# Kernel optimization log

Hardware: AMD Instinct MI355X
Metric: run time of the kernel (lower is better)

The kernel has to match this reference:

```python
import jax, jax.numpy as jnp
import numpy as np

NUM_ROI = 400
N_GRAPHS = 128
N_NODES = NUM_ROI * N_GRAPHS            # 51200
N_EDGES = N_NODES * 40                  # 2048000
EMB = [128, 128]
BN_EPS = 1e-5


def mish(x):
    return x * jnp.tanh(jax.nn.softplus(x))


def gcn_conv(x, row, col, ew, W, b, n_nodes):
    """PyG GCNConv: h = XW; add self-loops (w=1); sym-normalize; scatter-add; + bias."""
    h = x @ W                                            # [N, out]
    loops = jnp.arange(n_nodes, dtype=row.dtype)
    row_ = jnp.concatenate([row, loops])
    col_ = jnp.concatenate([col, loops])
    ew_ = jnp.concatenate([ew, jnp.ones((n_nodes,), ew.dtype)])
    deg = jax.ops.segment_sum(ew_, col_, num_segments=n_nodes)
    dinv = jnp.where(deg > 0, jax.lax.rsqrt(deg), 0.0)
    norm = dinv[row_] * ew_ * dinv[col_]                 # [E+N]
    msg = norm[:, None] * h[row_]                        # gather + scale
    out = jax.ops.segment_sum(msg, col_, num_segments=n_nodes)
    return out + b


def setup_inputs() -> dict:
    key = jax.random.key(0)
    ks = jax.random.split(key, 16)
    inp = {
        "x": jax.random.normal(ks[0], (N_NODES, NUM_ROI), jnp.float32),
        "edge_index": jax.random.randint(ks[1], (2, N_EDGES), 0, N_NODES, jnp.int64)
        if jax.config.jax_enable_x64 else jax.random.randint(ks[1], (2, N_EDGES), 0, N_NODES, jnp.int32),
        "edge_attr": jax.random.uniform(ks[2], (N_EDGES,), jnp.float32),
        "batch": jnp.repeat(jnp.arange(N_GRAPHS), NUM_ROI),
        "conv1_w": jax.random.normal(ks[3], (NUM_ROI, EMB[0]), jnp.float32) * 0.05,
        "conv1_b": jax.random.normal(ks[4], (EMB[0],), jnp.float32) * 0.05,
        "conv2_w": jax.random.normal(ks[5], (EMB[0], EMB[1]), jnp.float32) * 0.05,
        "conv2_b": jax.random.normal(ks[6], (EMB[1],), jnp.float32) * 0.05,
        "ro_w": jax.random.normal(ks[7], (EMB[1], 8), jnp.float32) * 0.05,
        "ro_b": jax.random.normal(ks[8], (8,), jnp.float32) * 0.05,
        "fc1_w": jax.random.normal(ks[9], (8 * NUM_ROI, NUM_ROI), jnp.float32) * 0.02,
        "fc1_b": jax.random.normal(ks[10], (NUM_ROI,), jnp.float32) * 0.02,
        "bn_gamma": jnp.ones((NUM_ROI,), jnp.float32),
        "bn_beta": jnp.zeros((NUM_ROI,), jnp.float32),
        "fc2_w": jax.random.normal(ks[11], (NUM_ROI, 2), jnp.float32) * 0.05,
        "fc2_b": jax.random.normal(ks[12], (2,), jnp.float32) * 0.05,
    }
    return inp


def reference(x, edge_index, edge_attr, batch,
              conv1_w, conv1_b, conv2_w, conv2_b,
              ro_w, ro_b, fc1_w, fc1_b, bn_gamma, bn_beta, fc2_w, fc2_b):
    n = x.shape[0]
    row, col = edge_index[0], edge_index[1]
    h = mish(gcn_conv(x, row, col, edge_attr, conv1_w, conv1_b, n))
    h = mish(gcn_conv(h, row, col, edge_attr, conv2_w, conv2_b, n))
    out = mish(h @ ro_w + ro_b)                          # [N, 8]
    feats = out.reshape(-1, NUM_ROI * 8)                 # [B, 3200]
    z = feats @ fc1_w + fc1_b                            # [B, 400]
    # BatchNorm1d (training mode: batch statistics, biased variance)
    mu = jnp.mean(z, axis=0)
    var = jnp.mean((z - mu) ** 2, axis=0)
    zn = (z - mu) * jax.lax.rsqrt(var + BN_EPS) * bn_gamma + bn_beta
    logits = mish(zn) @ fc2_w + fc2_b                    # [B, 2]
    return logits
```

## Files before the change

### kernel.cpp

```cpp
#include <hip/hip_runtime.h>
#include <hip/hip_fp16.h>
#include <math.h>

#define NN 51200
#define NE 2048000
#define F 128
#define NB 1000
#define EPB 2048
#define NBKT 200
#define ECAP 12288

typedef _Float16 half8 __attribute__((ext_vector_type(8)));
typedef float floatx4 __attribute__((ext_vector_type(4)));

__device__ __forceinline__ float mish_f(float x) {
  if (x > 20.0f) return x;
  float e = __expf(x);
  float w = 1.0f + e;
  w = w * w;
  return x * (w - 1.0f) / (w + 1.0f);
}

__global__ __launch_bounds__(256) void k_ic(const int* __restrict__ ei, unsigned* __restrict__ G,
                                            const float* __restrict__ W1, const float* __restrict__ W2,
                                            _Float16* __restrict__ Wt1, _Float16* __restrict__ Wt2,
                                            float* __restrict__ z) {
  int bid = blockIdx.x, t = threadIdx.x;
  if (bid < NB) {
    __shared__ unsigned hist[NBKT];
    for (int i = t; i < NBKT; i += 256) hist[i] = 0u;
    __syncthreads();
    int base = bid * EPB;
    for (int it = 0; it < EPB; it += 256) {
      int dst = ei[NE + base + it + t];
      atomicAdd(&hist[dst >> 8], 1u);
    }
    __syncthreads();
    for (int i = t; i < NBKT; i += 256) G[(size_t)i * NB + bid] = hist[i];
  } else {
    int idx = (bid - NB) * 256 + t;
    if (idx < 51200) {
      int k = idx >> 7, n = idx & 127;
      Wt1[n * 400 + k] = (_Float16)W1[idx];
      z[idx] = 0.0f;
    } else {
      int i2 = idx - 51200;
      int k = i2 >> 7, n = i2 & 127;
      Wt2[n * 128 + k] = (_Float16)W2[i2];
    }
  }
}

__global__ __launch_bounds__(64) void k_bscan(unsigned* __restrict__ G, unsigned* __restrict__ btot) {
  int b = blockIdx.x, l = threadIdx.x;
  unsigned base = (unsigned)l * 16;
  unsigned loc[16];
  unsigned s = 0;
#pragma unroll
  for (int i = 0; i < 16; ++i) {
    unsigned idx = base + i;
    unsigned x = (idx < NB) ? G[(size_t)b * NB + idx] : 0u;
    loc[i] = s;
    s += x;
  }
  unsigned run = s;
#pragma unroll
  for (int off = 1; off < 64; off <<= 1) {
    unsigned y = __shfl_up(run, off);
    if (l >= off) run += y;
  }
  unsigned excl = run - s;
#pragma unroll
  for (int i = 0; i < 16; ++i) {
    unsigned idx = base + i;
    if (idx < NB) G[(size_t)b * NB + idx] = excl + loc[i];
  }
  if (l == 63) btot[b] = run;
}

__global__ __launch_bounds__(256) void k_cscat(const int* __restrict__ ei, const float* __restrict__ ew,
                                               const unsigned* __restrict__ G,
                                               uint2* __restrict__ E) {
  __shared__ unsigned cur[NBKT];
  int blk = blockIdx.x, t = threadIdx.x;
  for (int i = t; i < NBKT; i += 256) cur[i] = (unsigned)i * ECAP + G[(size_t)i * NB + blk];
  __syncthreads();
  int base = blk * EPB;
  for (int it = 0; it < EPB; it += 256) {
    int e = base + it + t;
    int dst = ei[NE + e];
    int src = ei[e];
    float w = ew[e];
    unsigned pos = atomicAdd(&cur[dst >> 8], 1u);
    E[pos] = make_uint2((unsigned)src | ((unsigned)(dst & 255) << 16), __float_as_uint(w));
  }
}

__global__ __launch_bounds__(512) void k_fprep(const uint2* __restrict__ E, const unsigned* __restrict__ btot,
                                               int2* __restrict__ bounds, float* __restrict__ dinv,
                                               unsigned* __restrict__ csr) {
  __shared__ unsigned lc[256];
  __shared__ float ld[256];
  __shared__ int curs[256];
  __shared__ int ws4[4];
  __shared__ int starts[256];
  int b = blockIdx.x, t = threadIdx.x;
  if (t < 256) {
    lc[t] = 0u;
    ld[t] = 0.f;
  }
  __syncthreads();
  unsigned e0 = (unsigned)b * ECAP, e1 = e0 + btot[b];
  for (unsigned e = e0 + t; e < e1; e += 512) {
    uint2 v = E[e];
    unsigned node = (v.x >> 16) & 255u;
    atomicAdd(&lc[node], 1u);
    atomicAdd(&ld[node], __uint_as_float(v.y));
  }
  __syncthreads();
  if (t < 256) {
    int lane = t & 63, wid = t >> 6;
    int cv = (int)lc[t];
    int x = cv;
#pragma unroll
    for (int off = 1; off < 64; off <<= 1) {
      int y = __shfl_up(x, off);
      if (lane >= off) x += y;
    }
    if (lane == 63) ws4[wid] = x;
    __syncthreads();
    int woff = 0;
    for (int k = 0; k < wid; ++k) woff += ws4[k];
    int start = (int)e0 + woff + x - cv;
    bounds[b * 256 + t] = make_int2(start, start + cv);
    dinv[b * 256 + t] = rsqrtf(ld[t] + 1.0f);
    curs[t] = start;
    starts[t] = start;
  } else {
    __syncthreads();
  }
  __syncthreads();
  for (unsigned e = e0 + t; e < e1; e += 512) {
    uint2 v = E[e];
    unsigned node = (v.x >> 16) & 255u;
    unsigned src = v.x & 0xFFFFu;
    int p = atomicAdd(&curs[node], 1);
    unsigned pk = src | ((unsigned)__half_as_ushort(__float2half_rn(__uint_as_float(v.y))) << 16);
    csr[p] = pk;
  }
  (void)starts;
}

template <bool A_IS_F32>
__global__ __launch_bounds__(256) void k_gemm16(const void* __restrict__ Av,
                                                const _Float16* __restrict__ Wt,
                                                const float* __restrict__ dinv,
                                                __half* __restrict__ C, int K) {
  __shared__ _Float16 As[128][40];
  __shared__ _Float16 Bs[128][40];
  int t = threadIdx.x;
  int bm = blockIdx.x * 128;
  int w = t >> 6, l = t & 63, rr = l & 15, q = l >> 4;
  int si = t >> 1, sj = (t & 1) * 16;

  floatx4 acc[2][8];
#pragma unroll
  for (int a = 0; a < 2; ++a)
#pragma unroll
    for (int b = 0; b < 8; ++b) acc[a][b] = (floatx4){0.f, 0.f, 0.f, 0.f};

  for (int k0 = 0; k0 < K; k0 += 32) {
    if (A_IS_F32) {
      const float* A = (const float*)Av;
      half8 h0, h1;
      if (k0 + sj < K) {
        const float* ap = A + (size_t)(bm + si) * K + k0 + sj;
        float4 v0 = *(const float4*)(ap + 0);
        float4 v1 = *(const float4*)(ap + 4);
        float4 v2 = *(const float4*)(ap + 8);
        float4 v3 = *(const float4*)(ap + 12);
        h0 = (half8){(_Float16)v0.x, (_Float16)v0.y, (_Float16)v0.z, (_Float16)v0.w,
                     (_Float16)v1.x, (_Float16)v1.y, (_Float16)v1.z, (_Float16)v1.w};
        h1 = (half8){(_Float16)v2.x, (_Float16)v2.y, (_Float16)v2.z, (_Float16)v2.w,
                     (_Float16)v3.x, (_Float16)v3.y, (_Float16)v3.z, (_Float16)v3.w};
      } else {
        h0 = (half8){0, 0, 0, 0, 0, 0, 0, 0};
        h1 = h0;
      }
      *(half8*)&As[si][sj] = h0;
      *(half8*)&As[si][sj + 8] = h1;
    } else {
      const __half* A = (const __half*)Av;
      uint4 u0, u1;
      if (k0 + sj < K) {
        const __half* ap = A + (size_t)(bm + si) * K + k0 + sj;
        u0 = *(const uint4*)ap;
        u1 = *(const uint4*)(ap + 8);
      } else {
        u0 = make_uint4(0, 0, 0, 0);
        u1 = u0;
      }
      *(uint4*)&As[si][sj] = u0;
      *(uint4*)&As[si][sj + 8] = u1;
    }
    {
      uint4 u0, u1;
      if (k0 + sj < K) {
        const _Float16* wp = Wt + (size_t)si * K + k0 + sj;
        u0 = *(const uint4*)wp;
        u1 = *(const uint4*)(wp + 8);
      } else {
        u0 = make_uint4(0, 0, 0, 0);
        u1 = u0;
      }
      *(uint4*)&Bs[si][sj] = u0;
      *(uint4*)&Bs[si][sj + 8] = u1;
    }
    __syncthreads();

    half8 a0 = *(const half8*)&As[w * 32 + rr][q * 8];
    half8 a1 = *(const half8*)&As[w * 32 + 16 + rr][q * 8];
#pragma unroll
    for (int nt = 0; nt < 8; ++nt) {
      half8 b = *(const half8*)&Bs[nt * 16 + rr][q * 8];
      acc[0][nt] = __builtin_amdgcn_mfma_f32_16x16x32_f16(a0, b, acc[0][nt], 0, 0, 0);
      acc[1][nt] = __builtin_amdgcn_mfma_f32_16x16x32_f16(a1, b, acc[1][nt], 0, 0, 0);
    }
    __syncthreads();
  }
#pragma unroll
  for (int mt = 0; mt < 2; ++mt) {
    float dv[4];
#pragma unroll
    for (int r4 = 0; r4 < 4; ++r4) dv[r4] = dinv[bm + w * 32 + mt * 16 + q * 4 + r4];
#pragma unroll
    for (int nt = 0; nt < 8; ++nt)
#pragma unroll
      for (int r4 = 0; r4 < 4; ++r4) {
        int row = bm + w * 32 + mt * 16 + q * 4 + r4;
        C[(size_t)row * 128 + nt * 16 + rr] = __float2half(dv[r4] * acc[mt][nt][r4]);
      }
  }
}

__global__ __launch_bounds__(256) void k_agg(const __half2* __restrict__ h, const int2* __restrict__ bounds,
                                             const unsigned* __restrict__ csr, const float* __restrict__ dinv,
                                             const float* __restrict__ bias, __half2* __restrict__ out) {
  unsigned lane = threadIdx.x & 63u;
  int n = blockIdx.x * 4 + (threadIdx.x >> 6);
  float di = dinv[n];
  float2 self = __half22float2(h[((unsigned)n << 6) + lane]);
  float sx = 0.f, sy = 0.f;
  int2 bd = bounds[n];
  int p = __builtin_amdgcn_readfirstlane(bd.x);
  int p1 = __builtin_amdgcn_readfirstlane(bd.y);
  for (; p + 16 <= p1; p += 16) {
    unsigned c[16];
#pragma unroll
    for (int u = 0; u < 16; ++u) c[u] = csr[p + u];
    float2 f[16];
#pragma unroll
    for (int u = 0; u < 16; ++u) f[u] = __half22float2(h[((c[u] & 0xFFFFu) << 6) + lane]);
#pragma unroll
    for (int u = 0; u < 16; ++u) {
      float w = __half2float(__ushort_as_half((unsigned short)(c[u] >> 16)));
      sx += w * f[u].x;
      sy += w * f[u].y;
    }
  }
  for (; p + 4 <= p1; p += 4) {
    unsigned c[4];
#pragma unroll
    for (int u = 0; u < 4; ++u) c[u] = csr[p + u];
    float2 f[4];
#pragma unroll
    for (int u = 0; u < 4; ++u) f[u] = __half22float2(h[((c[u] & 0xFFFFu) << 6) + lane]);
#pragma unroll
    for (int u = 0; u < 4; ++u) {
      float w = __half2float(__ushort_as_half((unsigned short)(c[u] >> 16)));
      sx += w * f[u].x;
      sy += w * f[u].y;
    }
  }
  for (; p < p1; ++p) {
    unsigned c0 = csr[p];
    float2 f0 = __half22float2(h[((c0 & 0xFFFFu) << 6) + lane]);
    float w = __half2float(__ushort_as_half((unsigned short)(c0 >> 16)));
    sx += w * f0.x;
    sy += w * f0.y;
  }
  float2 bb = ((const float2*)bias)[lane];
  float ax = di * (sx + self.x) + bb.x;
  float ay = di * (sy + self.y) + bb.y;
  out[((unsigned)n << 6) + lane] = __floats2half2_rn(mish_f(ax), mish_f(ay));
}

__global__ __launch_bounds__(256) void k_agg2ro(const __half2* __restrict__ h, const int2* __restrict__ bounds,
                                                const unsigned* __restrict__ csr, const float* __restrict__ dinv,
                                                const float* __restrict__ bias, const float* __restrict__ rw,
                                                const float* __restrict__ rb, float* __restrict__ o8) {
  __shared__ float wl[128 * 8];
  int t = threadIdx.x;
  for (int i = t; i < 1024; i += 256) wl[i] = rw[i];
  __syncthreads();
  unsigned lane = t & 63u;
  int n = blockIdx.x * 4 + (t >> 6);
  float di = dinv[n];
  float2 self = __half22float2(h[((unsigned)n << 6) + lane]);
  float sx = 0.f, sy = 0.f;
  int2 bd = bounds[n];
  int p = __builtin_amdgcn_readfirstlane(bd.x);
  int p1 = __builtin_amdgcn_readfirstlane(bd.y);
  for (; p + 16 <= p1; p += 16) {
    unsigned c[16];
#pragma unroll
    for (int u = 0; u < 16; ++u) c[u] = csr[p + u];
    float2 f[16];
#pragma unroll
    for (int u = 0; u < 16; ++u) f[u] = __half22float2(h[((c[u] & 0xFFFFu) << 6) + lane]);
#pragma unroll
    for (int u = 0; u < 16; ++u) {
      float w = __half2float(__ushort_as_half((unsigned short)(c[u] >> 16)));
      sx += w * f[u].x;
      sy += w * f[u].y;
    }
  }
  for (; p + 4 <= p1; p += 4) {
    unsigned c[4];
#pragma unroll
    for (int u = 0; u < 4; ++u) c[u] = csr[p + u];
    float2 f[4];
#pragma unroll
    for (int u = 0; u < 4; ++u) f[u] = __half22float2(h[((c[u] & 0xFFFFu) << 6) + lane]);
#pragma unroll
    for (int u = 0; u < 4; ++u) {
      float w = __half2float(__ushort_as_half((unsigned short)(c[u] >> 16)));
      sx += w * f[u].x;
      sy += w * f[u].y;
    }
  }
  for (; p < p1; ++p) {
    unsigned c0 = csr[p];
    float2 f0 = __half22float2(h[((c0 & 0xFFFFu) << 6) + lane]);
    float w = __half2float(__ushort_as_half((unsigned short)(c0 >> 16)));
    sx += w * f0.x;
    sy += w * f0.y;
  }
  float2 bb = ((const float2*)bias)[lane];
  float m0 = mish_f(di * (sx + self.x) + bb.x);
  float m1 = mish_f(di * (sy + self.y) + bb.y);
  float p8[8];
#pragma unroll
  for (int k = 0; k < 8; ++k)
    p8[k] = m0 * wl[(2 * lane) * 8 + k] + m1 * wl[(2 * lane + 1) * 8 + k];
#pragma unroll
  for (int off = 1; off < 64; off <<= 1)
#pragma unroll
    for (int k = 0; k < 8; ++k) p8[k] += __shfl_xor(p8[k], off);
  if (lane < 8) o8[(size_t)n * 8 + lane] = mish_f(p8[lane] + rb[lane]);
}

__global__ __launch_bounds__(448) void k_fc1(const float* __restrict__ feats, const float* __restrict__ w,
                                             float* __restrict__ z) {
  __shared__ float fs[8][128];
  int t = threadIdx.x;
  int kc = blockIdx.x * 128;
  int g0 = blockIdx.y * 8;
  for (int i = t; i < 1024; i += 448) {
    int g = i >> 7, k = i & 127;
    fs[g][k] = feats[(size_t)(g0 + g) * 3200 + kc + k];
  }
  __syncthreads();
  if (t < 400) {
    float a[8];
#pragma unroll
    for (int g = 0; g < 8; ++g) a[g] = 0.0f;
    for (int k = 0; k < 128; ++k) {
      float wv = w[(size_t)(kc + k) * 400 + t];
#pragma unroll
      for (int g = 0; g < 8; ++g) a[g] += fs[g][k] * wv;
    }
#pragma unroll
    for (int g = 0; g < 8; ++g) atomicAdd(&z[(size_t)(g0 + g) * 400 + t], a[g]);
  }
}

__global__ __launch_bounds__(128) void k_bn(const float* __restrict__ z, const float* __restrict__ gamma,
                                            const float* __restrict__ beta, float* __restrict__ gs,
                                            float* __restrict__ gb) {
  int j = blockIdx.x;
  int b = threadIdx.x;
  float v = z[b * 400 + j];
  float s = v, s2 = v * v;
#pragma unroll
  for (int off = 1; off < 64; off <<= 1) {
    s += __shfl_xor(s, off);
    s2 += __shfl_xor(s2, off);
  }
  __shared__ float ls[2], ls2[2];
  if ((b & 63) == 0) {
    ls[b >> 6] = s;
    ls2[b >> 6] = s2;
  }
  __syncthreads();
  if (b == 0) {
    float mu = (ls[0] + ls[1]) * (1.0f / 128.0f);
    float var = (ls2[0] + ls2[1]) * (1.0f / 128.0f) - mu * mu;
    float rs = rsqrtf(var + 1e-5f);
    float g = gamma[j] * rs;
    gs[j] = g;
    gb[j] = beta[j] - mu * g;
  }
}

__global__ __launch_bounds__(256) void k_fc2(const float* __restrict__ z, const float* __restrict__ gs,
                                             const float* __restrict__ gb, const float* __restrict__ w2,
                                             const float* __restrict__ b2, float* __restrict__ out) {
  int bg = blockIdx.x;
  int t = threadIdx.x;
  float a0 = 0.f, a1 = 0.f;
  for (int j = t; j < 400; j += 256) {
    float zn = z[bg * 400 + j] * gs[j] + gb[j];
    float m = mish_f(zn);
    a0 += m * w2[j * 2];
    a1 += m * w2[j * 2 + 1];
  }
#pragma unroll
  for (int off = 1; off < 64; off <<= 1) {
    a0 += __shfl_xor(a0, off);
    a1 += __shfl_xor(a1, off);
  }
  __shared__ float s0[4], s1[4];
  if ((t & 63) == 0) {
    s0[t >> 6] = a0;
    s1[t >> 6] = a1;
  }
  __syncthreads();
  if (t == 0) {
    out[bg * 2 + 0] = b2[0] + s0[0] + s0[1] + s0[2] + s0[3];
    out[bg * 2 + 1] = b2[1] + s1[0] + s1[1] + s1[2] + s1[3];
  }
}

extern "C" void kernel_launch(void* const* d_in, const int* in_sizes, int n_in,
                              void* d_out, int out_size, void* d_ws, size_t ws_size,
                              hipStream_t stream) {
  (void)in_sizes; (void)n_in; (void)out_size; (void)ws_size;
  const float* x   = (const float*)d_in[0];
  const int*   ei  = (const int*)d_in[1];
  const float* ew  = (const float*)d_in[2];
  const float* c1w = (const float*)d_in[4];
  const float* c1b = (const float*)d_in[5];
  const float* c2w = (const float*)d_in[6];
  const float* c2b = (const float*)d_in[7];
  const float* rw  = (const float*)d_in[8];
  const float* rb  = (const float*)d_in[9];
  const float* f1w = (const float*)d_in[10];
  const float* bng = (const float*)d_in[12];
  const float* bnb = (const float*)d_in[13];
  const float* f2w = (const float*)d_in[14];
  const float* f2b = (const float*)d_in[15];
  float* out = (float*)d_out;

  char* ws = (char*)d_ws;
  size_t off = 0;
  auto alloc = [&](size_t bytes) {
    void* p = ws + off;
    off = (off + bytes + 255) & ~(size_t)255;
    return p;
  };
  float* dinv    = (float*)alloc((size_t)NN * 4);
  int2*  bounds  = (int2*)alloc((size_t)NN * 8);
  unsigned* G    = (unsigned*)alloc((size_t)NBKT * NB * 4);
  unsigned* btot = (unsigned*)alloc(NBKT * 4);
  unsigned* csr  = (unsigned*)alloc((size_t)NBKT * ECAP * 4);
  __half* A1     = (__half*)alloc((size_t)NN * F * 2);
  __half* B1     = (__half*)alloc((size_t)NN * F * 2);
  _Float16* Wt1  = (_Float16*)alloc((size_t)400 * 128 * 2);
  _Float16* Wt2  = (_Float16*)alloc((size_t)128 * 128 * 2);
  float* o8      = (float*)alloc((size_t)NN * 8 * 4);
  float* z       = (float*)alloc((size_t)128 * 400 * 4);
  float* gs      = (float*)alloc(400 * 4);
  float* gb      = (float*)alloc(400 * 4);

  uint2* E = (uint2*)A1;

  k_ic<<<NB + 264, 256, 0, stream>>>(ei, G, c1w, c2w, Wt1, Wt2, z);
  k_bscan<<<NBKT, 64, 0, stream>>>(G, btot);
  k_cscat<<<NB, 256, 0, stream>>>(ei, ew, G, E);
  k_fprep<<<NBKT, 512, 0, stream>>>(E, btot, bounds, dinv, csr);

  k_gemm16<true><<<NN / 128, 256, 0, stream>>>(x, Wt1, dinv, A1, 400);
  k_agg<<<NN / 4, 256, 0, stream>>>((const __half2*)A1, bounds, csr, dinv, c1b, (__half2*)B1);
  k_gemm16<false><<<NN / 128, 256, 0, stream>>>(B1, Wt2, dinv, A1, 128);
  k_agg2ro<<<NN / 4, 256, 0, stream>>>((const __half2*)A1, bounds, csr, dinv, c2b, rw, rb, o8);

  {
    dim3 g(25, 16);
    k_fc1<<<g, 448, 0, stream>>>(o8, f1w, z);
  }
  k_bn<<<400, 128, 0, stream>>>(z, bng, bnb, gs, gb);
  k_fc2<<<128, 256, 0, stream>>>(z, gs, gb, f2w, f2b, out);
}
```

Baseline: 409.5 us.

## Fuse bucket histogram, scan and scatter into one kernel using global atomic offsets

Replaces the three-kernel bucket partition (per-block histogram, per-bucket scan, scatter) with a single kernel. Each block stages its edges in shared memory, reserves space per bucket with global atomics on a zeroed counter array, then scatters. This removes two launches, the histogram matrix traffic and a second read of the edge arrays. The catch is that edge order within a bucket becomes nondeterministic, which changes the floating-point summation order. Separately, the readout weights are rearranged in shared memory as float2 per lane to avoid strided LDS reads.

```diff
diff --git a/kernel.cpp b/kernel.cpp
--- a/kernel.cpp
+++ b/kernel.cpp
@@ -21,22 +21,40 @@
   return x * (w - 1.0f) / (w + 1.0f);
 }
 
-__global__ __launch_bounds__(256) void k_ic(const int* __restrict__ ei, unsigned* __restrict__ G,
-                                            const float* __restrict__ W1, const float* __restrict__ W2,
-                                            _Float16* __restrict__ Wt1, _Float16* __restrict__ Wt2,
-                                            float* __restrict__ z) {
+__global__ __launch_bounds__(256) void k_icsort(const int* __restrict__ ei, const float* __restrict__ ew,
+                                                unsigned* __restrict__ gcnt, uint2* __restrict__ E,
+                                                const float* __restrict__ W1, const float* __restrict__ W2,
+                                                _Float16* __restrict__ Wt1, _Float16* __restrict__ Wt2,
+                                                float* __restrict__ z) {
   int bid = blockIdx.x, t = threadIdx.x;
   if (bid < NB) {
+    __shared__ uint2 ebuf[EPB];
+    __shared__ unsigned char bkt[EPB];
     __shared__ unsigned hist[NBKT];
+    __shared__ unsigned base[NBKT];
     for (int i = t; i < NBKT; i += 256) hist[i] = 0u;
     __syncthreads();
-    int base = bid * EPB;
+    int off0 = bid * EPB;
     for (int it = 0; it < EPB; it += 256) {
-      int dst = ei[NE + base + it + t];
-      atomicAdd(&hist[dst >> 8], 1u);
-    }
-    __syncthreads();
-    for (int i = t; i < NBKT; i += 256) G[(size_t)i * NB + bid] = hist[i];
+      int e = off0 + it + t;
+      int dst = ei[NE + e];
+      int src = ei[e];
+      float w = ew[e];
+      ebuf[it + t] = make_uint2((unsigned)src | ((unsigned)(dst & 255) << 16), __float_as_uint(w));
+      int b = dst >> 8;
+      bkt[it + t] = (unsigned char)b;
+      atomicAdd(&hist[b], 1u);
+    }
+    __syncthreads();
+    for (int i = t; i < NBKT; i += 256)
+      base[i] = (unsigned)i * ECAP + atomicAdd(&gcnt[i], hist[i]);
+    __syncthreads();
+    for (int it = 0; it < EPB; it += 256) {
+      int j = it + t;
+      unsigned b = bkt[j];
+      unsigned pos = atomicAdd(&base[b], 1u);
+      E[pos] = ebuf[j];
+    }
   } else {
     int idx = (bid - NB) * 256 + t;
     if (idx < 51200) {
@@ -51,51 +69,6 @@
   }
 }
 
-__global__ __launch_bounds__(64) void k_bscan(unsigned* __restrict__ G, unsigned* __restrict__ btot) {
-  int b = blockIdx.x, l = threadIdx.x;
-  unsigned base = (unsigned)l * 16;
-  unsigned loc[16];
-  unsigned s = 0;
-#pragma unroll
-  for (int i = 0; i < 16; ++i) {
-    unsigned idx = base + i;
-    unsigned x = (idx < NB) ? G[(size_t)b * NB + idx] : 0u;
-    loc[i] = s;
-    s += x;
-  }
-  unsigned run = s;
-#pragma unroll
-  for (int off = 1; off < 64; off <<= 1) {
-    unsigned y = __shfl_up(run, off);
-    if (l >= off) run += y;
-  }
-  unsigned excl = run - s;
-#pragma unroll
-  for (int i = 0; i < 16; ++i) {
-    unsigned idx = base + i;
-    if (idx < NB) G[(size_t)b * NB + idx] = excl + loc[i];
-  }
-  if (l == 63) btot[b] = run;
-}
-
-__global__ __launch_bounds__(256) void k_cscat(const int* __restrict__ ei, const float* __restrict__ ew,
-                                               const unsigned* __restrict__ G,
-                                               uint2* __restrict__ E) {
-  __shared__ unsigned cur[NBKT];
-  int blk = blockIdx.x, t = threadIdx.x;
-  for (int i = t; i < NBKT; i += 256) cur[i] = (unsigned)i * ECAP + G[(size_t)i * NB + blk];
-  __syncthreads();
-  int base = blk * EPB;
-  for (int it = 0; it < EPB; it += 256) {
-    int e = base + it + t;
-    int dst = ei[NE + e];
-    int src = ei[e];
-    float w = ew[e];
-    unsigned pos = atomicAdd(&cur[dst >> 8], 1u);
-    E[pos] = make_uint2((unsigned)src | ((unsigned)(dst & 255) << 16), __float_as_uint(w));
-  }
-}
-
 __global__ __launch_bounds__(512) void k_fprep(const uint2* __restrict__ E, const unsigned* __restrict__ btot,
                                                int2* __restrict__ bounds, float* __restrict__ dinv,
                                                unsigned* __restrict__ csr) {
@@ -103,7 +76,6 @@
   __shared__ float ld[256];
   __shared__ int curs[256];
   __shared__ int ws4[4];
-  __shared__ int starts[256];
   int b = blockIdx.x, t = threadIdx.x;
   if (t < 256) {
     lc[t] = 0u;
@@ -135,7 +107,6 @@
     bounds[b * 256 + t] = make_int2(start, start + cv);
     dinv[b * 256 + t] = rsqrtf(ld[t] + 1.0f);
     curs[t] = start;
-    starts[t] = start;
   } else {
     __syncthreads();
   }
@@ -148,7 +119,6 @@
     unsigned pk = src | ((unsigned)__half_as_ushort(__float2half_rn(__uint_as_float(v.y))) << 16);
     csr[p] = pk;
   }
-  (void)starts;
 }
 
 template <bool A_IS_F32>
@@ -299,9 +269,12 @@
                                                 const unsigned* __restrict__ csr, const float* __restrict__ dinv,
                                                 const float* __restrict__ bias, const float* __restrict__ rw,
                                                 const float* __restrict__ rb, float* __restrict__ o8) {
-  __shared__ float wl[128 * 8];
+  __shared__ float2 wl2[8][64];
   int t = threadIdx.x;
-  for (int i = t; i < 1024; i += 256) wl[i] = rw[i];
+  for (int i = t; i < 512; i += 256) {
+    int k = i >> 6, l = i & 63;
+    wl2[k][l] = make_float2(rw[(2 * l) * 8 + k], rw[(2 * l + 1) * 8 + k]);
+  }
   __syncthreads();
   unsigned lane = t & 63u;
   int n = blockIdx.x * 4 + (t >> 6);
@@ -351,8 +324,10 @@
   float m1 = mish_f(di * (sy + self.y) + bb.y);
   float p8[8];
 #pragma unroll
-  for (int k = 0; k < 8; ++k)
-    p8[k] = m0 * wl[(2 * lane) * 8 + k] + m1 * wl[(2 * lane + 1) * 8 + k];
+  for (int k = 0; k < 8; ++k) {
+    float2 wv = wl2[k][lane];
+    p8[k] = m0 * wv.x + m1 * wv.y;
+  }
 #pragma unroll
   for (int off = 1; off < 64; off <<= 1)
 #pragma unroll
@@ -471,8 +446,7 @@
   };
   float* dinv    = (float*)alloc((size_t)NN * 4);
   int2*  bounds  = (int2*)alloc((size_t)NN * 8);
-  unsigned* G    = (unsigned*)alloc((size_t)NBKT * NB * 4);
-  unsigned* btot = (unsigned*)alloc(NBKT * 4);
+  unsigned* gcnt = (unsigned*)alloc(NBKT * 4);
   unsigned* csr  = (unsigned*)alloc((size_t)NBKT * ECAP * 4);
   __half* A1     = (__half*)alloc((size_t)NN * F * 2);
   __half* B1     = (__half*)alloc((size_t)NN * F * 2);
@@ -485,10 +459,9 @@
 
   uint2* E = (uint2*)A1;
 
-  k_ic<<<NB + 264, 256, 0, stream>>>(ei, G, c1w, c2w, Wt1, Wt2, z);
-  k_bscan<<<NBKT, 64, 0, stream>>>(G, btot);
-  k_cscat<<<NB, 256, 0, stream>>>(ei, ew, G, E);
-  k_fprep<<<NBKT, 512, 0, stream>>>(E, btot, bounds, dinv, csr);
+  hipMemsetAsync(gcnt, 0, NBKT * 4, stream);
+  k_icsort<<<NB + 264, 256, 0, stream>>>(ei, ew, gcnt, E, c1w, c2w, Wt1, Wt2, z);
+  k_fprep<<<NBKT, 512, 0, stream>>>(E, gcnt, bounds, dinv, csr);
 
   k_gemm16<true><<<NN / 128, 256, 0, stream>>>(x, Wt1, dinv, A1, 400);
   k_agg<<<NN / 4, 256, 0, stream>>>((const __half2*)A1, bounds, csr, dinv, c1b, (__half2*)B1);
```

New measurement: 405.9 us. No clear change (-0.9%).
